# Performance work log

Measured on AMD Instinct MI355X. Metric: run time of the kernel, lower is better.

Reference implementation:

```python
import jax, jax.numpy as jnp
import numpy as np

N, LQ, D_MODEL, M_HEADS, P_POINTS, H_DIM, W_DIM = 8, 4096, 256, 8, 4, 64, 64


def setup_inputs() -> dict:
    key = jax.random.key(0)
    ks = jax.random.split(key, 9)
    d = D_MODEL
    scale = 1.0 / np.sqrt(d).astype(np.float32)
    return {
        "query": jax.random.normal(ks[0], (N, LQ, d), jnp.float32),
        "reference_points": jax.random.uniform(ks[1], (N, LQ, 2), jnp.float32),
        "input_flatten": jax.random.normal(ks[2], (N, H_DIM * W_DIM, d), jnp.float32),
        "H": H_DIM,
        "W": W_DIM,
        "Wv": jax.random.normal(ks[3], (d, d), jnp.float32) * scale,
        "bv": jnp.zeros((d,), jnp.float32),
        "Woff": jax.random.normal(ks[4], (M_HEADS * P_POINTS * 2, d), jnp.float32) * 0.01,
        "boff": jax.random.normal(ks[5], (M_HEADS * P_POINTS * 2,), jnp.float32) * 0.5,
        "Wa": jax.random.normal(ks[6], (M_HEADS * P_POINTS, d), jnp.float32) * 0.01,
        "ba": jnp.zeros((M_HEADS * P_POINTS,), jnp.float32),
        "Wo": jax.random.normal(ks[7], (d, d), jnp.float32) * scale,
        "bo": jnp.zeros((d,), jnp.float32),
    }


def _bilinear_sample(val, grid, H, W):
    # val: [B, D, H*W]; grid: [B, Lq, P, 2] in [-1, 1] (x, y); align_corners=False, zero padding.
    B, D, _ = val.shape
    _, Lq, P, _ = grid.shape
    x = (grid[..., 0] + 1.0) * (W * 0.5) - 0.5
    y = (grid[..., 1] + 1.0) * (H * 0.5) - 0.5
    x0 = jnp.floor(x)
    y0 = jnp.floor(y)
    x0i = x0.astype(jnp.int32)
    y0i = y0.astype(jnp.int32)
    wx1 = x - x0
    wy1 = y - y0
    out = jnp.zeros((B, D, Lq, P), val.dtype)
    for xi, wx in ((x0i, 1.0 - wx1), (x0i + 1, wx1)):
        for yi, wy in ((y0i, 1.0 - wy1), (y0i + 1, wy1)):
            valid = (xi >= 0) & (xi < W) & (yi >= 0) & (yi < H)
            idx = jnp.clip(yi, 0, H - 1) * W + jnp.clip(xi, 0, W - 1)  # [B, Lq, P]
            g = jnp.take_along_axis(val, idx.reshape(B, 1, Lq * P), axis=2).reshape(B, D, Lq, P)
            w = jnp.where(valid, wx * wy, 0.0)
            out = out + g * w[:, None]
    return out


def reference(query, reference_points, input_flatten, H, W, Wv, bv, Woff, boff, Wa, ba, Wo, bo):
    n, lq, d = query.shape
    m, p = M_HEADS, P_POINTS
    dh = d // m
    value = (input_flatten @ Wv.T + bv).reshape(n, H * W, m, dh)
    offsets = (query @ Woff.T + boff).reshape(n, lq, m, p, 2)
    attw = jax.nn.softmax((query @ Wa.T + ba).reshape(n, lq, m, p), axis=-1)
    normalizer = jnp.array([W, H], dtype=query.dtype)  # [W, H] order per torch code
    loc = reference_points[:, :, None, None, :] + offsets / normalizer
    grid = 2.0 * loc - 1.0  # [n, lq, m, p, 2]
    # value -> [n*m, dh, H*W] matching torch flatten(2).transpose(1,2).reshape
    val = jnp.transpose(value, (0, 2, 3, 1)).reshape(n * m, dh, H * W)
    grd = jnp.transpose(grid, (0, 2, 1, 3, 4)).reshape(n * m, lq, p, 2)
    samp = _bilinear_sample(val, grd, H, W)  # [n*m, dh, lq, p]
    aw = jnp.transpose(attw, (0, 2, 1, 3)).reshape(n * m, 1, lq, p)
    out = (samp * aw).sum(-1).reshape(n, m * dh, lq)
    out = jnp.transpose(out, (0, 2, 1))  # [n, lq, d]
    return out @ Wo.T + bo
```

## Files before the change

### kernel.cpp

```cpp
#include <hip/hip_runtime.h>
#include <math.h>

#define NB   8
#define LQN  4096
#define DM   256
#define MH   8
#define PP   4
#define HH   64
#define WW   64
#define LG   128
#define PW   67
#define PPIX (PW*PW)
#define ASTR 40

typedef __bf16 bf16x8 __attribute__((ext_vector_type(8)));
typedef float  f32x4  __attribute__((ext_vector_type(4)));
typedef unsigned short us8 __attribute__((ext_vector_type(8)));

__device__ __forceinline__ unsigned short f2bf(float f) {
    unsigned u = __float_as_uint(f);
    u += 0x7FFFu + ((u >> 16) & 1u);
    return (unsigned short)(u >> 16);
}
__device__ __forceinline__ float bf2f(unsigned short b) {
    return __uint_as_float((unsigned)b << 16);
}

__device__ __forceinline__ void gl2lds16(const unsigned short* g, unsigned short* l) {
    __builtin_amdgcn_global_load_lds(
        (const __attribute__((address_space(1))) void*)g,
        (__attribute__((address_space(3))) void*)l,
        16, 0, 0);
}

__global__ __launch_bounds__(256, 2)
void dual_gemm(const float* __restrict__ Ain, const float* __restrict__ Aq,
               const unsigned short* __restrict__ Wvh,
               const unsigned short* __restrict__ Wcath,
               const float* __restrict__ bv, const float* __restrict__ bcat,
               unsigned short* __restrict__ valueP,
               unsigned short* __restrict__ logitsB) {
    constexpr int K = 256;
    __shared__ unsigned short sA[2][128 * ASTR];
    __shared__ unsigned short sB[2][4096];

    const int t    = threadIdx.x;
    const int blk  = blockIdx.x;
    const bool isVal = (blk < 512);

    const float* A; const unsigned short* B; const float* bias;
    int brow, bcol;
    if (isVal) { A = Ain; B = Wvh;   bias = bv;   brow = (blk >> 1) * 128; bcol = (blk & 1) * 128; }
    else       { A = Aq;  B = Wcath; bias = bcat; brow = (blk - 512) * 128; bcol = 0; }

    const int ar  = t >> 1;
    const int as_ = (t & 1) * 16;
    const float* aG = A + (size_t)(brow + ar) * K + as_;
    const int abase = ar * ASTR + as_;

    const unsigned short* bG = B + (size_t)(bcol + (t >> 2)) * K + (t & 3) * 8;
    const size_t brs64 = (size_t)64 * K;

    const int l   = t & 63;
    const int wid = t >> 6;
    const int wr  = wid >> 1, wc = wid & 1;
    const int fr  = l & 15,   kq = l >> 4;

    f32x4 acc[4][4] = {};
    float4 va[4];

#define LOAD_A(k0)                                                     \
    {  _Pragma("unroll")                                               \
       for (int j = 0; j < 4; ++j)                                     \
           va[j] = *(const float4*)(aG + (k0) + j * 4); }

#define STAGE_B(buf, k0)                                               \
    {  gl2lds16(bG + (k0),         &sB[buf][t * 8]);                   \
       gl2lds16(bG + (k0) + brs64, &sB[buf][2048 + t * 8]); }

#define STAGE_A(buf)                                                   \
    {  _Pragma("unroll")                                               \
       for (int g = 0; g < 2; ++g) {                                   \
           us8 Hv;                                                     \
           _Pragma("unroll")                                           \
           for (int j = 0; j < 2; ++j) {                               \
               const float4 v = va[g * 2 + j];                         \
               Hv[j*4+0] = f2bf(v.x); Hv[j*4+1] = f2bf(v.y);           \
               Hv[j*4+2] = f2bf(v.z); Hv[j*4+3] = f2bf(v.w);           \
           }                                                           \
           *(us8*)&sA[buf][abase + g * 8] = Hv;                        \
       } }

    LOAD_A(0);
    STAGE_B(0, 0);
    STAGE_A(0);

    for (int ks = 0; ks < K / 32; ++ks) {
        __syncthreads();
        const int cur = ks & 1, nxt = cur ^ 1;
        const bool more = (ks + 1 < K / 32);
        if (more) {
            LOAD_A((ks + 1) * 32);
            STAGE_B(nxt, (ks + 1) * 32);
        }

        bf16x8 ah[4], bf_[4];
#pragma unroll
        for (int m = 0; m < 4; ++m)
            ah[m] = *(const bf16x8*)&sA[cur][(wr * 64 + m * 16 + fr) * ASTR + kq * 8];
#pragma unroll
        for (int n = 0; n < 4; ++n)
            bf_[n] = *(const bf16x8*)&sB[cur][(wc * 64 + n * 16 + fr) * 32 + kq * 8];

#pragma unroll
        for (int m = 0; m < 4; ++m)
#pragma unroll
            for (int n = 0; n < 4; ++n)
                acc[m][n] = __builtin_amdgcn_mfma_f32_16x16x32_bf16(
                    ah[m], bf_[n], acc[m][n], 0, 0, 0);

        if (more) STAGE_A(nxt);
    }
#undef LOAD_A
#undef STAGE_B
#undef STAGE_A

#pragma unroll
    for (int n = 0; n < 4; ++n) {
        const int colg = bcol + wc * 64 + n * 16 + fr;
        const float bs = bias[colg];
#pragma unroll
        for (int m = 0; m < 4; ++m) {
            const int rowg = brow + wr * 64 + m * 16 + kq * 4;
#pragma unroll
            for (int j = 0; j < 4; ++j) {
                const float v = acc[m][n][j] + bs;
                const int row = rowg + j;
                if (isVal) {
                    const int nb_ = row >> 12;
                    const int pix = row & 4095;
                    const int y   = pix >> 6, x = pix & 63;
                    const size_t addr =
                        ((size_t)nb_ * PPIX + (size_t)(y + 1) * PW + (x + 1)) * DM + colg;
                    valueP[addr] = f2bf(v);
                } else {
                    logitsB[(size_t)row * LG + colg] = f2bf(v);
                }
            }
        }
    }
}

__global__ __launch_bounds__(256, 2)
void gemm_bf16_nt(const unsigned short* __restrict__ A,
                  const unsigned short* __restrict__ B,
                  const float* __restrict__ bias, float* __restrict__ C,
                  int M, int N, int K) {
    __shared__ unsigned short sA[2][4096];
    __shared__ unsigned short sB[2][4096];

    const int t    = threadIdx.x;
    const int brow = blockIdx.x * 128;
    const int bcol = blockIdx.y * 128;

    const unsigned short* aG = A + (size_t)(brow + (t >> 2)) * K + (t & 3) * 8;
    const unsigned short* bG = B + (size_t)(bcol + (t >> 2)) * K + (t & 3) * 8;
    const size_t rs64 = (size_t)64 * K;

    const int l   = t & 63;
    const int wid = t >> 6;
    const int wr  = wid >> 1, wc = wid & 1;
    const int fr  = l & 15,   kq = l >> 4;

    f32x4 acc[4][4] = {};
    const int NK = K / 32;

    gl2lds16(aG,        &sA[0][t * 8]);
    gl2lds16(aG + rs64, &sA[0][2048 + t * 8]);
    gl2lds16(bG,        &sB[0][t * 8]);
    gl2lds16(bG + rs64, &sB[0][2048 + t * 8]);

    for (int ks = 0; ks < NK; ++ks) {
        __syncthreads();
        if (ks + 1 < NK) {
            const int nb = (ks & 1) ^ 1;
            const int k0 = (ks + 1) * 32;
            gl2lds16(aG + k0,        &sA[nb][t * 8]);
            gl2lds16(aG + k0 + rs64, &sA[nb][2048 + t * 8]);
            gl2lds16(bG + k0,        &sB[nb][t * 8]);
            gl2lds16(bG + k0 + rs64, &sB[nb][2048 + t * 8]);
        }
        const int buf = ks & 1;
        bf16x8 af[4], bfr[4];
#pragma unroll
        for (int m = 0; m < 4; ++m)
            af[m]  = *(const bf16x8*)&sA[buf][(wr * 64 + m * 16 + fr) * 32 + kq * 8];
#pragma unroll
        for (int n = 0; n < 4; ++n)
            bfr[n] = *(const bf16x8*)&sB[buf][(wc * 64 + n * 16 + fr) * 32 + kq * 8];
#pragma unroll
        for (int m = 0; m < 4; ++m)
#pragma unroll
            for (int n = 0; n < 4; ++n)
                acc[m][n] = __builtin_amdgcn_mfma_f32_16x16x32_bf16(
                    af[m], bfr[n], acc[m][n], 0, 0, 0);
    }

#pragma unroll
    for (int n = 0; n < 4; ++n) {
        const int colg = bcol + wc * 64 + n * 16 + fr;
        const float bs = bias[colg];
#pragma unroll
        for (int m = 0; m < 4; ++m) {
            const int rowg = brow + wr * 64 + m * 16 + kq * 4;
#pragma unroll
            for (int j = 0; j < 4; ++j)
                C[(size_t)(rowg + j) * N + colg] = acc[m][n][j] + bs;
        }
    }
}

__global__ __launch_bounds__(256)
void prep_kernel(const float* __restrict__ Wv, const float* __restrict__ Wo,
                 const float* __restrict__ Woff, const float* __restrict__ Wa,
                 const float* __restrict__ boff, const float* __restrict__ ba,
                 unsigned short* __restrict__ Wvh, unsigned short* __restrict__ Woh,
                 unsigned short* __restrict__ Wcath, float* __restrict__ bcat,
                 unsigned short* __restrict__ valueP) {
    const int i = blockIdx.x * 256 + threadIdx.x;
    if (i < 65536) {
        Wvh[i] = f2bf(Wv[i]);
    } else if (i < 131072) {
        const int j = i - 65536;
        Woh[j] = f2bf(Wo[j]);
    } else if (i < 163840) {
        const int j = i - 131072, n = j >> 8, k = j & 255;
        const float v = (n < 64) ? Woff[n * 256 + k]
                                 : ((n < 96) ? Wa[(n - 64) * 256 + k] : 0.f);
        Wcath[j] = f2bf(v);
    } else if (i < 163968) {
        const int n = i - 163840;
        bcat[n] = (n < 64) ? boff[n] : ((n < 96) ? ba[n - 64] : 0.f);
    } else if (i < 163968 + 201216) {
        const int j   = i - 163968;
        const int c4  = j & 63;
        const int pix = j >> 6;
        const int n   = pix / 393;
        const int r   = pix - n * 393;
        int x, y;
        if (r < 201) {
            const int q = r / 67;
            y = (q == 0) ? 0 : (q == 1 ? 65 : 66);
            x = r - q * 67;
        } else {
            const int q = r - 201;
            y = 1 + q / 3;
            const int s = q - (q / 3) * 3;
            x = (s == 0) ? 0 : (s == 1 ? 65 : 66);
        }
        const size_t addr = ((size_t)n * PPIX + (size_t)y * PW + x) * DM + c4 * 4;
        *(ushort4*)&valueP[addr] = make_ushort4(0, 0, 0, 0);
    }
}

__global__ __launch_bounds__(256)
void sample_kernel(const float* __restrict__ refp,
                   const unsigned short* __restrict__ valueP,
                   const unsigned short* __restrict__ logitsB,
                   unsigned short* __restrict__ sampledH) {
    const int vb   = (blockIdx.x & 7) * 1024 + (blockIdx.x >> 3);
    const int wid  = threadIdx.x >> 6;
    const int b    = vb * 4 + wid;
    const int n    = b >> 12;
    const int lane = threadIdx.x & 63;

    const int tp  = lane & 31;
    const int pm  = tp >> 2, ppt = tp & 3;
    const unsigned short* lg = logitsB + (size_t)b * LG;

    const float rx = refp[(size_t)b * 2 + 0];
    const float ry = refp[(size_t)b * 2 + 1];
    const float ox = bf2f(lg[pm * 8 + ppt * 2 + 0]);
    const float oy = bf2f(lg[pm * 8 + ppt * 2 + 1]);
    const float la = bf2f(lg[64 + tp]);

    const float x = fminf(fmaxf(fmaf(rx, (float)WW, ox) - 0.5f, -1.0f), 64.0f);
    const float y = fminf(fmaxf(fmaf(ry, (float)HH, oy) - 0.5f, -1.0f), 64.0f);

    float mx = fmaxf(la, __shfl_xor(la, 1));
    mx = fmaxf(mx, __shfl_xor(mx, 2));
    const float e = __expf(la - mx);
    float den = e + __shfl_xor(e, 1);
    den += __shfl_xor(den, 2);
    const float w = e / den;

    const int half = lane >> 5;
    const int c8   = lane & 31;
    const int mh   = c8 >> 2;
    const unsigned short* vbase = valueP + (size_t)n * (PPIX * DM) + c8 * 8;

    float accv[8] = {};
#pragma unroll
    for (int p = 0; p < PP; ++p) {
        const int   sl = mh * PP + p;
        const float xp = __shfl(x, sl);
        const float yp = __shfl(y, sl);
        const float wp = __shfl(w, sl);

        const float x0f = floorf(xp), y0f = floorf(yp);
        const int   x0 = (int)x0f,   y0 = (int)y0f;
        const float wx1 = xp - x0f,  wy1 = yp - y0f;
        const float wy  = half ? wy1 : (1.f - wy1);
        const float wA  = wp * wy * (1.f - wx1);
        const float wB  = wp * wy * wx1;

        const unsigned short* p0 =
            vbase + (size_t)((y0 + 1 + half) * PW + (x0 + 1)) * DM;
        const us8 gA = *(const us8*)(p0);
        const us8 gB = *(const us8*)(p0 + DM);
#pragma unroll
        for (int j = 0; j < 8; ++j) {
            accv[j] = fmaf(wA, bf2f(gA[j]), accv[j]);
            accv[j] = fmaf(wB, bf2f(gB[j]), accv[j]);
        }
    }

#pragma unroll
    for (int j = 0; j < 8; ++j)
        accv[j] += __shfl_xor(accv[j], 32);

    if (half == 0) {
        us8 o;
#pragma unroll
        for (int j = 0; j < 8; ++j) o[j] = f2bf(accv[j]);
        *(us8*)&sampledH[(size_t)b * DM + c8 * 8] = o;
    }
}

extern "C" void kernel_launch(void* const* d_in, const int* in_sizes, int n_in,
                              void* d_out, int out_size, void* d_ws, size_t ws_size,
                              hipStream_t stream) {
    const float* query  = (const float*)d_in[0];
    const float* refp   = (const float*)d_in[1];
    const float* inputf = (const float*)d_in[2];
    const float* Wv   = (const float*)d_in[5];
    const float* bv   = (const float*)d_in[6];
    const float* Woff = (const float*)d_in[7];
    const float* boff = (const float*)d_in[8];
    const float* Wa   = (const float*)d_in[9];
    const float* ba   = (const float*)d_in[10];
    const float* Wo   = (const float*)d_in[11];
    const float* bo   = (const float*)d_in[12];
    float* out = (float*)d_out;

    const int Mrows = NB * LQN;

    unsigned short* sampledH = (unsigned short*)d_ws;
    unsigned short* valueP   = sampledH + (size_t)Mrows * DM;
    unsigned short* logitsB  = valueP   + (size_t)NB * PPIX * DM;
    unsigned short* Wvh      = logitsB  + (size_t)Mrows * LG;
    unsigned short* Woh      = Wvh      + 65536;
    unsigned short* Wcath    = Woh      + 65536;
    float*          bcat     = (float*)(Wcath + 32768);

    prep_kernel<<<1427, 256, 0, stream>>>(Wv, Wo, Woff, Wa, boff, ba,
                                          Wvh, Woh, Wcath, bcat, valueP);

    dual_gemm<<<768, 256, 0, stream>>>(inputf, query, Wvh, Wcath, bv, bcat,
                                       valueP, logitsB);

    sample_kernel<<<Mrows / 4, 256, 0, stream>>>(refp, valueP, logitsB, sampledH);

    {
        dim3 g(Mrows / 128, 2);
        gemm_bf16_nt<<<g, 256, 0, stream>>>(sampledH, Woh, bo, out,
                                            Mrows, DM, 256);
    }
}
```

Before: 66.91 us.

## Stage fp32 A tiles via async global-to-LDS loads and vectorize GEMM epilogues

The dual GEMM now copies the fp32 activation tile straight into LDS with global_load_lds, using an XOR swizzle, instead of loading to registers and converting to bf16 before storing. Conversion to bf16 moves to the LDS read side, just before the MFMA. The MFMA operands are swapped in both GEMMs so each lane holds four consecutive output columns, which allows vectorized 4-wide stores and bias loads in the epilogues. This removes register staging and scattered scalar stores, at the cost of twice the LDS footprint for A and extra conversion work inside the inner loop.

```diff
diff --git a/kernel.cpp b/kernel.cpp
--- a/kernel.cpp
+++ b/kernel.cpp
@@ -11,11 +11,11 @@
 #define LG   128
 #define PW   67
 #define PPIX (PW*PW)
-#define ASTR 40
 
 typedef __bf16 bf16x8 __attribute__((ext_vector_type(8)));
 typedef float  f32x4  __attribute__((ext_vector_type(4)));
 typedef unsigned short us8 __attribute__((ext_vector_type(8)));
+typedef unsigned short us4 __attribute__((ext_vector_type(4)));
 
 __device__ __forceinline__ unsigned short f2bf(float f) {
     unsigned u = __float_as_uint(f);
@@ -26,7 +26,7 @@
     return __uint_as_float((unsigned)b << 16);
 }
 
-__device__ __forceinline__ void gl2lds16(const unsigned short* g, unsigned short* l) {
+__device__ __forceinline__ void gl2lds16(const void* g, unsigned short* l) {
     __builtin_amdgcn_global_load_lds(
         (const __attribute__((address_space(1))) void*)g,
         (__attribute__((address_space(3))) void*)l,
@@ -41,7 +41,7 @@
                unsigned short* __restrict__ valueP,
                unsigned short* __restrict__ logitsB) {
     constexpr int K = 256;
-    __shared__ unsigned short sA[2][128 * ASTR];
+    __shared__ unsigned short sA[2][8192];
     __shared__ unsigned short sB[2][4096];
 
     const int t    = threadIdx.x;
@@ -50,13 +50,15 @@
 
     const float* A; const unsigned short* B; const float* bias;
     int brow, bcol;
-    if (isVal) { A = Ain; B = Wvh;   bias = bv;   brow = (blk >> 1) * 128; bcol = (blk & 1) * 128; }
-    else       { A = Aq;  B = Wcath; bias = bcat; brow = (blk - 512) * 128; bcol = 0; }
-
-    const int ar  = t >> 1;
-    const int as_ = (t & 1) * 16;
-    const float* aG = A + (size_t)(brow + ar) * K + as_;
-    const int abase = ar * ASTR + as_;
+    if (isVal) { A = Ain; B = Wvh;   bias = bv;
+                 brow = (blk >> 1) * 128; bcol = (blk & 1) * 128; }
+    else       { A = Aq;  B = Wcath; bias = bcat;
+                 brow = (blk - 512) * 128; bcol = 0; }
+
+    const int arow = t >> 3;
+    const int acsw = (t & 7) ^ (arow & 7);
+    const float* aG = A + (size_t)(brow + arow) * K + acsw * 4;
+    const size_t aIss = (size_t)32 * K;
 
     const unsigned short* bG = B + (size_t)(bcol + (t >> 2)) * K + (t & 3) * 8;
     const size_t brs64 = (size_t)64 * K;
@@ -67,47 +69,38 @@
     const int fr  = l & 15,   kq = l >> 4;
 
     f32x4 acc[4][4] = {};
-    float4 va[4];
-
-#define LOAD_A(k0)                                                     \
-    {  _Pragma("unroll")                                               \
-       for (int j = 0; j < 4; ++j)                                     \
-           va[j] = *(const float4*)(aG + (k0) + j * 4); }
-
-#define STAGE_B(buf, k0)                                               \
-    {  gl2lds16(bG + (k0),         &sB[buf][t * 8]);                   \
+
+#define STAGE(buf, k0)                                                   \
+    {  gl2lds16(aG + (k0),            &sA[buf][t * 8]);                  \
+       gl2lds16(aG + (k0) + aIss,     &sA[buf][2048 + t * 8]);           \
+       gl2lds16(aG + (k0) + 2 * aIss, &sA[buf][4096 + t * 8]);           \
+       gl2lds16(aG + (k0) + 3 * aIss, &sA[buf][6144 + t * 8]);           \
+       gl2lds16(bG + (k0),         &sB[buf][t * 8]);                     \
        gl2lds16(bG + (k0) + brs64, &sB[buf][2048 + t * 8]); }
 
-#define STAGE_A(buf)                                                   \
-    {  _Pragma("unroll")                                               \
-       for (int g = 0; g < 2; ++g) {                                   \
-           us8 Hv;                                                     \
-           _Pragma("unroll")                                           \
-           for (int j = 0; j < 2; ++j) {                               \
-               const float4 v = va[g * 2 + j];                         \
-               Hv[j*4+0] = f2bf(v.x); Hv[j*4+1] = f2bf(v.y);           \
-               Hv[j*4+2] = f2bf(v.z); Hv[j*4+3] = f2bf(v.w);           \
-           }                                                           \
-           *(us8*)&sA[buf][abase + g * 8] = Hv;                        \
-       } }
-
-    LOAD_A(0);
-    STAGE_B(0, 0);
-    STAGE_A(0);
-
+    STAGE(0, 0);
+
+    const int fr7 = fr & 7;
     for (int ks = 0; ks < K / 32; ++ks) {
         __syncthreads();
-        const int cur = ks & 1, nxt = cur ^ 1;
-        const bool more = (ks + 1 < K / 32);
-        if (more) {
-            LOAD_A((ks + 1) * 32);
-            STAGE_B(nxt, (ks + 1) * 32);
-        }
-
-        bf16x8 ah[4], bf_[4];
-#pragma unroll
-        for (int m = 0; m < 4; ++m)
-            ah[m] = *(const bf16x8*)&sA[cur][(wr * 64 + m * 16 + fr) * ASTR + kq * 8];
+        if (ks + 1 < K / 32) STAGE((ks & 1) ^ 1, (ks + 1) * 32);
+        const int cur = ks & 1;
+
+        bf16x8 af[4], bf_[4];
+#pragma unroll
+        for (int m = 0; m < 4; ++m) {
+            const int row = wr * 64 + m * 16 + fr;
+            const int u0  = row * 8 + ((kq * 2 + 0) ^ fr7);
+            const int u1  = row * 8 + ((kq * 2 + 1) ^ fr7);
+            const f32x4 a0 = *(const f32x4*)&sA[cur][u0 * 8];
+            const f32x4 a1 = *(const f32x4*)&sA[cur][u1 * 8];
+            us8 av;
+            av[0] = f2bf(a0[0]); av[1] = f2bf(a0[1]);
+            av[2] = f2bf(a0[2]); av[3] = f2bf(a0[3]);
+            av[4] = f2bf(a1[0]); av[5] = f2bf(a1[1]);
+            av[6] = f2bf(a1[2]); av[7] = f2bf(a1[3]);
+            af[m] = *(bf16x8*)&av;
+        }
 #pragma unroll
         for (int n = 0; n < 4; ++n)
             bf_[n] = *(const bf16x8*)&sB[cur][(wc * 64 + n * 16 + fr) * 32 + kq * 8];
@@ -117,45 +110,41 @@
 #pragma unroll
             for (int n = 0; n < 4; ++n)
                 acc[m][n] = __builtin_amdgcn_mfma_f32_16x16x32_bf16(
-                    ah[m], bf_[n], acc[m][n], 0, 0, 0);
-
-        if (more) STAGE_A(nxt);
-    }
-#undef LOAD_A
-#undef STAGE_B
-#undef STAGE_A
-
-#pragma unroll
-    for (int n = 0; n < 4; ++n) {
-        const int colg = bcol + wc * 64 + n * 16 + fr;
-        const float bs = bias[colg];
-#pragma unroll
-        for (int m = 0; m < 4; ++m) {
-            const int rowg = brow + wr * 64 + m * 16 + kq * 4;
-#pragma unroll
-            for (int j = 0; j < 4; ++j) {
-                const float v = acc[m][n][j] + bs;
-                const int row = rowg + j;
-                if (isVal) {
-                    const int nb_ = row >> 12;
-                    const int pix = row & 4095;
-                    const int y   = pix >> 6, x = pix & 63;
-                    const size_t addr =
-                        ((size_t)nb_ * PPIX + (size_t)(y + 1) * PW + (x + 1)) * DM + colg;
-                    valueP[addr] = f2bf(v);
-                } else {
-                    logitsB[(size_t)row * LG + colg] = f2bf(v);
-                }
-            }
+                    bf_[n], af[m], acc[m][n], 0, 0, 0);
+    }
+#undef STAGE
+
+#pragma unroll
+    for (int m = 0; m < 4; ++m) {
+        const int row = brow + wr * 64 + m * 16 + fr;
+        size_t rbase;
+        if (isVal) {
+            const int nb_ = row >> 12;
+            const int pix = row & 4095;
+            const int y   = pix >> 6, x = pix & 63;
+            rbase = ((size_t)nb_ * PPIX + (size_t)(y + 1) * PW + (x + 1)) * DM;
+        } else {
+            rbase = (size_t)row * LG;
+        }
+#pragma unroll
+        for (int n = 0; n < 4; ++n) {
+            const int colq = bcol + wc * 64 + n * 16 + kq * 4;
+            const float4 bs = *(const float4*)&bias[colq];
+            us4 o;
+            o[0] = f2bf(acc[m][n][0] + bs.x);
+            o[1] = f2bf(acc[m][n][1] + bs.y);
+            o[2] = f2bf(acc[m][n][2] + bs.z);
+            o[3] = f2bf(acc[m][n][3] + bs.w);
+            *(us4*)&(isVal ? valueP : logitsB)[rbase + colq] = o;
         }
     }
 }
 
 __global__ __launch_bounds__(256, 2)
-void gemm_bf16_nt(const unsigned short* __restrict__ A,
-                  const unsigned short* __restrict__ B,
-                  const float* __restrict__ bias, float* __restrict__ C,
-                  int M, int N, int K) {
+void gemm_out(const unsigned short* __restrict__ A,
+              const unsigned short* __restrict__ B,
+              const float* __restrict__ bias, float* __restrict__ C) {
+    constexpr int K = 256, N = DM;
     __shared__ unsigned short sA[2][4096];
     __shared__ unsigned short sB[2][4096];
 
@@ -203,19 +192,20 @@
 #pragma unroll
             for (int n = 0; n < 4; ++n)
                 acc[m][n] = __builtin_amdgcn_mfma_f32_16x16x32_bf16(
-                    af[m], bfr[n], acc[m][n], 0, 0, 0);
-    }
-
-#pragma unroll
-    for (int n = 0; n < 4; ++n) {
-        const int colg = bcol + wc * 64 + n * 16 + fr;
-        const float bs = bias[colg];
-#pragma unroll
-        for (int m = 0; m < 4; ++m) {
-            const int rowg = brow + wr * 64 + m * 16 + kq * 4;
-#pragma unroll
-            for (int j = 0; j < 4; ++j)
-                C[(size_t)(rowg + j) * N + colg] = acc[m][n][j] + bs;
+                    bfr[n], af[m], acc[m][n], 0, 0, 0);
+    }
+
+#pragma unroll
+    for (int m = 0; m < 4; ++m) {
+        const int row = brow + wr * 64 + m * 16 + fr;
+#pragma unroll
+        for (int n = 0; n < 4; ++n) {
+            const int colq = bcol + wc * 64 + n * 16 + kq * 4;
+            const float4 bs = *(const float4*)&bias[colq];
+            float4 o;
+            o.x = acc[m][n][0] + bs.x; o.y = acc[m][n][1] + bs.y;
+            o.z = acc[m][n][2] + bs.z; o.w = acc[m][n][3] + bs.w;
+            *(float4*)&C[(size_t)row * N + colq] = o;
         }
     }
 }
@@ -372,8 +362,7 @@
     sample_kernel<<<Mrows / 4, 256, 0, stream>>>(refp, valueP, logitsB, sampledH);
 
     {
-        dim3 g(Mrows / 128, 2);
-        gemm_bf16_nt<<<g, 256, 0, stream>>>(sampledH, Woh, bo, out,
-                                            Mrows, DM, 256);
-    }
-}
+        dim3 g(Mrows / 128, DM / 128);
+        gemm_out<<<g, 256, 0, stream>>>(sampledH, Woh, bo, out);
+    }
+}
```

After: 67.32 us. Within noise of the previous version (+0.6%).
